# Performance work log

Measured on AMD Instinct MI355X. Metric: run time of the kernel, lower is better.

Reference implementation:

```python
import jax, jax.numpy as jnp
import numpy as np

N, C_IN, C_OUT, T, V = 128, 64, 64, 128, 25
GROUPS, K = 8, 3
REL = C_IN // 8  # rel_reduction=8, in_channels>16


def setup_inputs() -> dict:
    key = jax.random.key(0)
    ks = jax.random.split(key, 16)
    f = lambda k, sh, s=0.05: (jax.random.normal(k, sh) * s).astype(jnp.float32)
    return {
        "x0": jax.random.normal(ks[0], (N, C_IN, T, V), jnp.float32),
        "DecoupleA": f(ks[1], (K, GROUPS, V, V), 0.2),
        "A": f(ks[2], (K, V, V), 0.2),
        "alpha": jnp.full((1,), 0.5, jnp.float32),
        "w1": f(ks[3], (K, REL, C_IN)), "b1": f(ks[4], (K, REL)),
        "w2": f(ks[5], (K, REL, C_IN)), "b2": f(ks[6], (K, REL)),
        "w3": f(ks[7], (K, C_OUT, C_IN)), "b3": f(ks[8], (K, C_OUT)),
        "w4": f(ks[9], (K, C_OUT, REL)), "b4": f(ks[10], (K, C_OUT)),
        "Linear_weight": f(ks[11], (C_IN, C_OUT * K)),
        "Linear_bias": f(ks[12], (1, C_OUT * K, 1, 1)),
        "bn0_gamma": jnp.ones((C_OUT * K,), jnp.float32),
        "bn0_beta": jnp.zeros((C_OUT * K,), jnp.float32),
        "ens_w": f(ks[13], (C_OUT, 2 * C_OUT)), "ens_b": f(ks[14], (C_OUT,)),
        "bn_gamma": jnp.full((C_OUT,), 1e-6, jnp.float32),
        "bn_beta": jnp.zeros((C_OUT,), jnp.float32),
    }


def _bn(x, gamma, beta, eps=1e-5):
    # training-mode BatchNorm2d over NCHW: stats over (N, T, V)
    mu = x.mean(axis=(0, 2, 3), keepdims=True)
    var = x.var(axis=(0, 2, 3), keepdims=True)
    return (x - mu) * jax.lax.rsqrt(var + eps) * gamma[None, :, None, None] + beta[None, :, None, None]


def _norm_adj(A):
    # torch: D = A.sum(dim=rows) -> column sums; A @ diag(1/(D+1e-3)) scales columns
    d = A.sum(axis=-2)  # [..., V] column sums
    return A * (1.0 / (d + 0.001))[..., None, :]


def reference(x0, DecoupleA, A, alpha, w1, b1, w2, b2, w3, b3, w4, b4,
              Linear_weight, Linear_bias, bn0_gamma, bn0_beta, ens_w, ens_b,
              bn_gamma, bn_beta):
    n, c_in, t, v = x0.shape
    k, g = DecoupleA.shape[0], DecoupleA.shape[1]
    c_out = w3.shape[1]
    # DecoupleA.repeat(1, out_channels//groups, 1, 1) == tile along channel dim
    learn_A = jnp.tile(DecoupleA, (1, c_out // g, 1, 1))  # [K, C_OUT, V, V]
    norm_A = _norm_adj(learn_A)
    # decoupled linear path
    x = jnp.einsum('nctv,cd->ndtv', x0, Linear_weight) + Linear_bias
    x = _bn(x, bn0_gamma, bn0_beta)
    x = x.reshape(n, k, c_out, t, v)
    x = jnp.einsum('nkctv,kcvw->nctw', x, norm_A)  # [n, C_OUT, t, v]
    # CTRGC branches (conv-then-mean over T == mean-then-1x1 since conv is linear)
    xm = x0.mean(axis=2)  # [n, c_in, v]
    y = jnp.zeros((n, c_out, t, v), x0.dtype)
    for i in range(k):
        x1 = jnp.einsum('ncv,rc->nrv', xm, w1[i]) + b1[i][:, None]
        x2 = jnp.einsum('ncv,rc->nrv', xm, w2[i]) + b2[i][:, None]
        diff = jnp.tanh(x1[:, :, :, None] - x2[:, :, None, :])        # [n, rel, u, w]
        att = jnp.einsum('nruw,or->nouw', diff, w4[i]) + b4[i][None, :, None, None]
        att = att * alpha[0] + A[i][None, None]                        # [n, C_OUT, u, w]
        x3 = jnp.einsum('nctv,oc->notv', x0, w3[i]) + b3[i][None, :, None, None]
        y = y + jnp.einsum('ncuv,nctu->nctv', att, x3)
    cat = jnp.concatenate([x, y], axis=1)                              # [n, 2*C_OUT, t, v]
    out = jnp.einsum('nctv,oc->notv', cat, ens_w) + ens_b[None, :, None, None]
    out = _bn(out, bn_gamma, bn_beta)
    out = out + x0  # down is identity since in_channels == out_channels
    return jax.nn.relu(out)
```

## Files before the change

kernel.cpp:

```cpp
#include <hip/hip_runtime.h>
#include <cstddef>
#include <cstring>

typedef _Float16 h8 __attribute__((ext_vector_type(8)));
typedef _Float16 h4v __attribute__((ext_vector_type(4)));
typedef float f4 __attribute__((ext_vector_type(4)));
typedef unsigned int u32;
typedef unsigned short u16;

#define MTOT 409600.0f

#define DO_XM  15360000
#define DO_GP  15564800
#define DO_GR  16613376

#define WS_OB16 0
#define WS_ATT  13631488
#define WS_ATTB 23461888
#define WS_BN2P 23666688
#define WS_PAR  23827456
#define WS_CSN  23828000

#define ATT_H 27262976
#define NAB_H 47595520
#define WA_H  47622144
#define W3_H  47634432
#define EW_H  47646720

#define LDS_DYN 116736

__global__ __launch_bounds__(512) void k_gram(const float* __restrict__ x0,
                                              float* __restrict__ gp,
                                              const float* __restrict__ DA,
                                              const float* __restrict__ w3,
                                              const float* __restrict__ ensw,
                                              float* __restrict__ wsF) {
  int bid = blockIdx.x, tid = threadIdx.x;
  if (bid >= 256) {
    int pb = bid - 256;
    _Float16* wsH = (_Float16*)wsF;
    if (pb < 3) {
      if (tid < 200) {
        int k = pb, g = tid / 25, w = tid % 25;
        const float* base = DA + (k * 8 + g) * 625 + w;
        float s = 0.f;
        for (int v = 0; v < 25; v++) s += base[v * 25];
        float inv = 1.0f / (s + 0.001f);
        wsF[WS_CSN + k * 200 + g * 25 + w] = s * inv;
        _Float16* dst = wsH + NAB_H + (size_t)((k * 8 + g) * 32 + w) * 32;
        for (int v = 0; v < 25; v++) dst[v] = (_Float16)(base[v * 25] * inv);
        for (int v = 25; v < 32; v++) dst[v] = (_Float16)0.f;
      }
    } else if (pb == 3) {
      for (int idx = tid; idx < 5376; idx += 512) {
        int kg = idx / 224, r = idx % 224;
        int w = 25 + r / 32, v = r & 31;
        wsH[NAB_H + (size_t)(kg * 32 + w) * 32 + v] = (_Float16)0.f;
      }
    } else if (pb < 12) {
      int i0 = (pb - 4) * 1536;
      for (int i = tid; i < 1536; i += 512)
        wsH[W3_H + i0 + i] = (_Float16)w3[i0 + i];
    } else {
      int i0 = (pb - 12) * 2048;
      for (int i = tid; i < 2048; i += 512)
        wsH[EW_H + i0 + i] = (_Float16)ensw[i0 + i];
    }
    return;
  }
  __shared__ _Float16 Xs[64 * 128];
  char* smb = (char*)Xs;
  int n = bid >> 1, sh = bid & 1;
  int base = sh * 1536;
  int niter = sh ? 13 : 12;
  const float* xb = x0 + (size_t)n * 204800;
  int wid = tid >> 6, lane = tid & 63, l15 = lane & 15, l4 = lane >> 4;
  int ca = (wid & 3) * 16;
  int jb0 = (wid >> 2) * 2;
  f4 acc[2] = {{0.f, 0.f, 0.f, 0.f}, {0.f, 0.f, 0.f, 0.f}};
  int sc = tid >> 3, scol = (tid & 7) * 16;
  int swz = (sc & 7) << 4;
  for (int it = 0; it < niter; ++it) {
    int s0 = base + it * 128;
    __syncthreads();
    const float* src = xb + sc * 3200 + s0 + scol;
#pragma unroll
    for (int j = 0; j < 4; ++j) {
      float4 f = *(const float4*)(src + j * 4);
      h4v hv = {(_Float16)f.x, (_Float16)f.y, (_Float16)f.z, (_Float16)f.w};
      *(h4v*)(smb + sc * 256 + (((scol + j * 4) * 2) ^ swz)) = hv;
    }
    __syncthreads();
#pragma unroll
    for (int kk = 0; kk < 4; ++kk) {
      int kb = kk * 64 + l4 * 16;
      int arow = ca + l15;
      h8 af = *(const h8*)(smb + arow * 256 + (kb ^ ((arow & 7) << 4)));
#pragma unroll
      for (int j = 0; j < 2; ++j) {
        int brow = (jb0 + j) * 16 + l15;
        h8 bf = *(const h8*)(smb + brow * 256 + (kb ^ ((brow & 7) << 4)));
        acc[j] = __builtin_amdgcn_mfma_f32_16x16x32_f16(af, bf, acc[j], 0, 0, 0);
      }
    }
  }
  float* o = gp + (size_t)bid * 4096;
#pragma unroll
  for (int j = 0; j < 2; ++j)
#pragma unroll
    for (int q = 0; q < 4; ++q)
      o[(ca + l4 * 4 + q) * 64 + (jb0 + j) * 16 + l15] = acc[j][q];
}

__global__ __launch_bounds__(256) void k_gred(float* __restrict__ dsc) {
  int bid = blockIdx.x, tid = threadIdx.x;
  if (bid < 16) {
    int idx = bid * 256 + tid;
    const float* gp = dsc + DO_GP;
    float s0 = 0.f, s1 = 0.f, s2 = 0.f, s3 = 0.f;
    for (int b = 0; b < 256; b += 4) {
      s0 += gp[(size_t)b * 4096 + idx];
      s1 += gp[(size_t)(b + 1) * 4096 + idx];
      s2 += gp[(size_t)(b + 2) * 4096 + idx];
      s3 += gp[(size_t)(b + 3) * 4096 + idx];
    }
    dsc[DO_GR + idx] = (s0 + s1) + (s2 + s3);
  } else {
    __shared__ float red[64][5];
    int c = tid >> 2, j = tid & 3;
    float s = 0.f;
    for (int nn = j; nn < 128; nn += 4) {
      const float* xmp = dsc + DO_XM + (size_t)(nn * 64 + c) * 25;
      for (int v = 0; v < 25; ++v) s += xmp[v];
    }
    red[c][j] = s;
    __syncthreads();
    if (j == 0)
      dsc[DO_GR + 4096 + c] = 128.f * (red[c][0] + red[c][1] + red[c][2] + red[c][3]);
  }
}

__global__ __launch_bounds__(256) void k_xm(const float* __restrict__ x0,
                                            float* __restrict__ dsc) {
  __shared__ float red[8][32];
  int bid = blockIdx.x;
  int n = bid >> 6, c = bid & 63;
  int tid = threadIdx.x;
  int tq = tid >> 5, v = tid & 31;
  const float* xb = x0 + (size_t)(n * 64 + c) * 3200;
  float s = 0.f;
  if (v < 25) {
    for (int j = 0; j < 16; j++) s += xb[(tq + 8 * j) * 25 + v];
  }
  red[tq][v] = s;
  __syncthreads();
  if (tq == 0 && v < 25) {
    float tot = 0.f;
#pragma unroll
    for (int q = 0; q < 8; q++) tot += red[q][v];
    dsc[DO_XM + (size_t)(n * 64 + c) * 25 + v] = tot * (1.0f / 128.0f);
  }
}

__global__ __launch_bounds__(256) void k_bnstat(const float* __restrict__ dsc,
                                                const float* __restrict__ Lw,
                                                const float* __restrict__ g0,
                                                const float* __restrict__ b0,
                                                float* __restrict__ wsF) {
  __shared__ float Gsh[64 * 66];
  __shared__ float Ly[64][17];
  __shared__ float part[16][17];
  __shared__ float a1L[16];
  int bid = blockIdx.x, tid = threadIdx.x;
  int d0 = bid * 16, dl = tid >> 4, r = tid & 15, d = d0 + dl;
  for (int idx = tid; idx < 4096; idx += 256)
    Gsh[(idx >> 6) * 66 + (idx & 63)] = dsc[DO_GR + idx];
  for (int idx = tid; idx < 1024; idx += 256)
    Ly[idx >> 4][idx & 15] = Lw[(idx >> 4) * 192 + d0 + (idx & 15)];
  __syncthreads();
  float acc = 0.f;
#pragma unroll
  for (int cc = 0; cc < 4; ++cc) {
    int c = r * 4 + cc;
    float h = 0.f;
    for (int c2 = 0; c2 < 64; ++c2) h += Gsh[c * 66 + c2] * Ly[c2][dl];
    acc += Ly[c][dl] * h;
  }
  part[dl][r] = acc;
  __syncthreads();
  if (r == 0) {
    float ex2 = 0.f;
#pragma unroll
    for (int i = 0; i < 16; ++i) ex2 += part[dl][i];
    ex2 *= (1.0f / MTOT);
    float mu = 0.f;
    for (int c = 0; c < 64; ++c) mu += dsc[DO_GR + 4096 + c] * Ly[c][dl];
    mu *= (1.0f / MTOT);
    float var = ex2 - mu * mu;
    float a1 = g0[d] * rsqrtf(var + 1e-5f);
    float b1c = b0[d] - a1 * mu;
    wsF[WS_PAR + 128 + d] = a1;
    wsF[WS_PAR + 320 + d] = b1c;
    a1L[dl] = a1;
  }
  __syncthreads();
  _Float16* wsH = (_Float16*)wsF;
  int k = d >> 6, cg = d & 63;
  float a1v = a1L[dl];
#pragma unroll
  for (int j = 0; j < 4; ++j) {
    int e = r * 4 + j;
    wsH[WA_H + k * 4096 + cg * 64 + e] = (_Float16)(a1v * Lw[e * 192 + d]);
  }
}

__global__ __launch_bounds__(256) void k_att(const float* __restrict__ dsc,
    const float* __restrict__ w1, const float* __restrict__ b1,
    const float* __restrict__ w2, const float* __restrict__ b2,
    const float* __restrict__ w4, const float* __restrict__ b4,
    const float* __restrict__ Ag, const float* __restrict__ alpha,
    const float* __restrict__ b3, float* __restrict__ wsF) {
  __shared__ float xms[1600];
  __shared__ float x1s[200];
  __shared__ float x2s[200];
  __shared__ float Td[5000];
  int bid = blockIdx.x, tid = threadIdx.x;
  int n = bid / 3, i = bid % 3;
  for (int idx = tid; idx < 1600; idx += 256)
    xms[idx] = dsc[DO_XM + (size_t)n * 1600 + idx];
  __syncthreads();
  for (int idx = tid; idx < 400; idx += 256) {
    int r = (idx % 200) / 25, u = idx % 25;
    const float* wv = (idx < 200 ? w1 : w2) + (i * 8 + r) * 64;
    float acc = (idx < 200 ? b1 : b2)[i * 8 + r];
    for (int c = 0; c < 64; c++) acc += xms[c * 25 + u] * wv[c];
    if (idx < 200) x1s[r * 25 + u] = acc; else x2s[r * 25 + u] = acc;
  }
  __syncthreads();
  for (int idx = tid; idx < 5000; idx += 256) {
    int r = idx / 625, u = (idx % 625) / 25, w = idx % 25;
    Td[idx] = tanhf(x1s[r * 25 + u] - x2s[r * 25 + w]);
  }
  __syncthreads();
  float al = alpha[0];
  u32* attW = (u32*)wsF;
  for (int p = tid; p < 1600; p += 256) {
    int o = p / 25, w = p % 25;
    float w4r[8];
#pragma unroll
    for (int r = 0; r < 8; r++) w4r[r] = w4[(i * 64 + o) * 8 + r];
    float b4v = b4[i * 64 + o];
    const float* AgW = Ag + i * 625 + w;
    float asum = 0.f;
    size_t rowH = (size_t)ATT_H + ((size_t)((n * 3 + i) * 64 + o) * 25 + w) * 32;
    u32* row = attW + rowH / 2;
    for (int up = 0; up < 16; ++up) {
      u32 word = 0;
#pragma unroll
      for (int h = 0; h < 2; ++h) {
        int u = up * 2 + h;
        float v = 0.f;
        if (u < 25) {
          float acc = b4v;
#pragma unroll
          for (int r = 0; r < 8; r++) acc += w4r[r] * Td[r * 625 + u * 25 + w];
          v = al * acc + AgW[u * 25];
          asum += v;
        }
        union { _Float16 hf; u16 b; } cv;
        cv.hf = (_Float16)v;
        word |= ((u32)cv.b) << (16 * h);
      }
      row[up] = word;
    }
    atomicAdd(&wsF[WS_ATTB + (size_t)n * 1600 + p], b3[i * 64 + o] * asum);
  }
}

__device__ __forceinline__ void stageX(const float* __restrict__ xn, char* sm, int tid) {
  for (int uu = tid; uu < 6400; uu += 1024) {
    int cg = uu & 15, s = uu >> 4;
    int c0 = cg * 4;
    const float* p = xn + c0 * 3200 + s;
    float a = p[0], b = p[3200], c = p[6400], d = p[9600];
    h4v hv = {(_Float16)a, (_Float16)b, (_Float16)c, (_Float16)d};
    *(h4v*)(sm + s * 128 + ((c0 * 2) ^ ((s & 7) << 4))) = hv;
  }
}
__device__ __forceinline__ void zeroHpads(char* sm, int tid) {
  for (int idx = tid; idx < 7168; idx += 1024) {
    int c = idx / 112, r = idx % 112;
    int t = r / 7, u = 25 + r % 7;
    int hs = (((t & 3) ^ ((c >> 2) & 3)) << 4);
    *(_Float16*)(sm + 51200 + c * 1024 + t * 64 + ((u * 2) ^ hs)) = (_Float16)0.f;
  }
}
__device__ __forceinline__ void gemm64(const _Float16* __restrict__ Aw, char* sm,
                                       int mt, int nt0, int nt1, int lane) {
  int l15 = lane & 15, l4 = lane >> 4;
  h8 a0 = *(const h8*)(Aw + (mt * 16 + l15) * 64 + l4 * 8);
  h8 a1 = *(const h8*)(Aw + (mt * 16 + l15) * 64 + 32 + l4 * 8);
  int s = nt0 * 16 + l15;
  int t = s / 25, u = s - t * 25;
  int hsc = ((mt * 4 + l4) & 3) << 4;
  for (int nt = nt0; nt < nt1; ++nt) {
    int sw = (s & 7) << 4;
    const char* rb = sm + s * 128;
    h8 b0 = *(const h8*)(rb + ((l4 * 16) ^ sw));
    h8 b1 = *(const h8*)(rb + ((64 + l4 * 16) ^ sw));
    f4 acc = {0.f, 0.f, 0.f, 0.f};
    acc = __builtin_amdgcn_mfma_f32_16x16x32_f16(a0, b0, acc, 0, 0, 0);
    acc = __builtin_amdgcn_mfma_f32_16x16x32_f16(a1, b1, acc, 0, 0, 0);
    int hs = ((t & 3) << 4) ^ hsc;
    char* wb = sm + 51200 + (mt * 16 + l4 * 4) * 1024 + t * 64 + ((u * 2) ^ hs);
#pragma unroll
    for (int q = 0; q < 4; ++q)
      *(_Float16*)(wb + q * 1024) = (_Float16)acc[q];
    s += 16;
    u += 16;
    if (u >= 25) { u -= 25; ++t; }
  }
}

__global__ __launch_bounds__(1024, 4) void kAB(const float* __restrict__ x0,
                                               float* ws,
                                               const float* __restrict__ ensb) {
  extern __shared__ char sm[];
  __shared__ float redS[128];
  __shared__ float attBs[1600];
  __shared__ float cbS[1600];
  const _Float16* wsH = (const _Float16*)ws;
  int tid = threadIdx.x, bid = blockIdx.x;
  int lb = (bid & 7) * 128 + (bid >> 3);
  int n = lb >> 3, tile = lb & 7;
  int wid = tid >> 6, lane = tid & 63, l15 = lane & 15, l4 = lane >> 4;
  int mt = wid & 3, q4 = wid >> 2, g = wid & 7;
  int nt0 = q4 ? 1 + 6 * q4 : 0;
  int nt1 = q4 ? nt0 + 6 : 7;
  if (tid < 128) redS[tid] = 0.f;
  for (int idx = tid; idx < 1600; idx += 1024)
    attBs[idx] = ws[WS_ATTB + (size_t)n * 1600 + idx];
  for (int idx = tid; idx < 1600; idx += 1024) {
    int c = idx / 25, w = idx - c * 25;
    int gg = c & 7;
    float s = 0.f;
#pragma unroll
    for (int k = 0; k < 3; ++k)
      s += ws[WS_PAR + 320 + k * 64 + c] * ws[WS_CSN + k * 200 + gg * 25 + w];
    cbS[idx] = s;
  }
  stageX(x0 + (size_t)n * 204800 + tile * 400, sm, tid);
  zeroHpads(sm, tid);
  __syncthreads();
  f4 accx[4][2], accy[4][2];
#pragma unroll
  for (int a = 0; a < 4; a++)
#pragma unroll
    for (int b = 0; b < 2; b++) {
      accx[a][b] = (f4){0.f, 0.f, 0.f, 0.f};
      accy[a][b] = (f4){0.f, 0.f, 0.f, 0.f};
    }
  for (int k = 0; k < 3; ++k) {
    gemm64(wsH + WA_H + k * 4096, sm, mt, nt0, nt1, lane);
    __syncthreads();
#pragma unroll
    for (int mt2 = 0; mt2 < 4; ++mt2) {
      int c = mt2 * 16 + wid;
      int hs = (((l15 & 3) ^ ((c >> 2) & 3)) << 4);
      h8 aH = *(const h8*)(sm + 51200 + c * 1024 + l15 * 64 + ((l4 * 16) ^ hs));
#pragma unroll
      for (int nt2 = 0; nt2 < 2; ++nt2) {
        const _Float16* nb = wsH + NAB_H +
            (size_t)((k * 8 + g) * 32 + nt2 * 16 + l15) * 32 + l4 * 8;
        accx[mt2][nt2] = __builtin_amdgcn_mfma_f32_16x16x32_f16(
            aH, *(const h8*)nb, accx[mt2][nt2], 0, 0, 0);
      }
    }
    __syncthreads();
  }
  for (int i = 0; i < 3; ++i) {
    gemm64(wsH + W3_H + i * 4096, sm, mt, nt0, nt1, lane);
    __syncthreads();
#pragma unroll
    for (int mt2 = 0; mt2 < 4; ++mt2) {
      int c = mt2 * 16 + wid;
      int hs = (((l15 & 3) ^ ((c >> 2) & 3)) << 4);
      h8 aX = *(const h8*)(sm + 51200 + c * 1024 + l15 * 64 + ((l4 * 16) ^ hs));
#pragma unroll
      for (int nt2 = 0; nt2 < 2; ++nt2) {
        int v = nt2 * 16 + l15;
        int vc = v < 25 ? v : 0;
        const _Float16* ab = wsH + ATT_H +
            ((size_t)((n * 3 + i) * 64 + c) * 25 + vc) * 32 + l4 * 8;
        accy[mt2][nt2] = __builtin_amdgcn_mfma_f32_16x16x32_f16(
            aX, *(const h8*)ab, accy[mt2][nt2], 0, 0, 0);
      }
    }
    __syncthreads();
  }
#pragma unroll
  for (int mt2 = 0; mt2 < 4; ++mt2) {
    int c = mt2 * 16 + wid;
#pragma unroll
    for (int nt2 = 0; nt2 < 2; ++nt2) {
      int w = nt2 * 16 + l15;
      if (w < 25) {
        float cbv = cbS[c * 25 + w];
        float abv = attBs[c * 25 + w];
#pragma unroll
        for (int q = 0; q < 4; ++q) {
          int t = l4 * 4 + q;
          int s = t * 25 + w;
          int sw = (s & 7) << 4;
          *(_Float16*)(sm + s * 256 + ((c * 2) ^ sw)) =
              (_Float16)(accx[mt2][nt2][q] + cbv);
          *(_Float16*)(sm + s * 256 + (((64 + c) * 2) ^ sw)) =
              (_Float16)(accy[mt2][nt2][q] + abv);
        }
      }
    }
  }
  __syncthreads();
  h8 ea[4];
#pragma unroll
  for (int ks = 0; ks < 4; ++ks)
    ea[ks] = *(const h8*)(wsH + EW_H + (mt * 16 + l15) * 128 + ks * 32 + l4 * 8);
  float eb[4];
#pragma unroll
  for (int q = 0; q < 4; ++q) eb[q] = ensb[mt * 16 + l4 * 4 + q];
  float lsum[4] = {0.f, 0.f, 0.f, 0.f}, lss[4] = {0.f, 0.f, 0.f, 0.f};
  u16* ob16 = (u16*)ws;
  for (int nt = nt0; nt < nt1; ++nt) {
    int s = nt * 16 + l15;
    int sw = (s & 7) << 4;
    f4 acc = {0.f, 0.f, 0.f, 0.f};
#pragma unroll
    for (int ks = 0; ks < 4; ++ks) {
      h8 b = *(const h8*)(sm + s * 256 + (((ks * 32 + l4 * 8) * 2) ^ sw));
      acc = __builtin_amdgcn_mfma_f32_16x16x32_f16(ea[ks], b, acc, 0, 0, 0);
    }
    size_t ob = (size_t)n * 204800 + (size_t)tile * 400 + s;
#pragma unroll
    for (int q = 0; q < 4; ++q) {
      int o = mt * 16 + l4 * 4 + q;
      union { _Float16 hf; u16 b; } cv;
      cv.hf = (_Float16)(acc[q] + eb[q]);
      ob16[ob + (size_t)o * 3200] = cv.b;
      float val = (float)cv.hf;
      lsum[q] += val;
      lss[q] += val * val;
    }
  }
#pragma unroll
  for (int q = 0; q < 4; ++q) {
#pragma unroll
    for (int d = 1; d < 16; d <<= 1) {
      lsum[q] += __shfl_xor(lsum[q], d);
      lss[q] += __shfl_xor(lss[q], d);
    }
  }
  if (l15 == 0) {
#pragma unroll
    for (int q = 0; q < 4; ++q) {
      int o = mt * 16 + l4 * 4 + q;
      atomicAdd(&redS[o], lsum[q]);
      atomicAdd(&redS[64 + o], lss[q]);
    }
  }
  __syncthreads();
  if (tid < 64) {
    ws[WS_BN2P + (size_t)bid * 128 + tid * 2] = redS[tid];
    ws[WS_BN2P + (size_t)bid * 128 + tid * 2 + 1] = redS[64 + tid];
  }
}

__global__ __launch_bounds__(256) void k_bn2(const float* __restrict__ g2,
                                             const float* __restrict__ b2,
                                             float* __restrict__ ws) {
  __shared__ float rs[256], rss[256];
  int o = blockIdx.x, tid = threadIdx.x;
  float s = 0.f, ss = 0.f;
  for (int b = tid; b < 1024; b += 256) {
    s += ws[WS_BN2P + (size_t)b * 128 + o * 2];
    ss += ws[WS_BN2P + (size_t)b * 128 + o * 2 + 1];
  }
  rs[tid] = s; rss[tid] = ss;
  __syncthreads();
  for (int st = 128; st > 0; st >>= 1) {
    if (tid < st) { rs[tid] += rs[tid + st]; rss[tid] += rss[tid + st]; }
    __syncthreads();
  }
  if (tid == 0) {
    float mu = rs[0] / MTOT;
    float var = rss[0] / MTOT - mu * mu;
    float a2 = g2[o] * rsqrtf(var + 1e-5f);
    ws[WS_PAR + o] = a2;
    ws[WS_PAR + 64 + o] = b2[o] - a2 * mu;
  }
}

__global__ __launch_bounds__(256) void k_final(const float* __restrict__ x0,
                                               const float* __restrict__ ws,
                                               float* __restrict__ dout) {
  size_t g = (size_t)blockIdx.x * 256 + threadIdx.x;
  h4v p = reinterpret_cast<const h4v*>(ws)[g];
  float4 x = reinterpret_cast<const float4*>(x0)[g];
  int o = (int)((g * 4 / 3200) & 63);
  float a2 = ws[WS_PAR + o], bc = ws[WS_PAR + 64 + o];
  float4 r;
  r.x = fmaxf(fmaf(a2, (float)p[0], bc) + x.x, 0.f);
  r.y = fmaxf(fmaf(a2, (float)p[1], bc) + x.y, 0.f);
  r.z = fmaxf(fmaf(a2, (float)p[2], bc) + x.z, 0.f);
  r.w = fmaxf(fmaf(a2, (float)p[3], bc) + x.w, 0.f);
  reinterpret_cast<float4*>(dout)[g] = r;
}

extern "C" void kernel_launch(void* const* d_in, const int* in_sizes, int n_in,
                              void* d_out, int out_size, void* d_ws, size_t ws_size,
                              hipStream_t stream) {
  const float* x0    = (const float*)d_in[0];
  const float* DA    = (const float*)d_in[1];
  const float* Ag    = (const float*)d_in[2];
  const float* alpha = (const float*)d_in[3];
  const float* w1    = (const float*)d_in[4];
  const float* b1    = (const float*)d_in[5];
  const float* w2    = (const float*)d_in[6];
  const float* b2    = (const float*)d_in[7];
  const float* w3    = (const float*)d_in[8];
  const float* b3    = (const float*)d_in[9];
  const float* w4    = (const float*)d_in[10];
  const float* b4    = (const float*)d_in[11];
  const float* Lw    = (const float*)d_in[12];
  const float* g0    = (const float*)d_in[14];
  const float* b0    = (const float*)d_in[15];
  const float* ensw  = (const float*)d_in[16];
  const float* ensb  = (const float*)d_in[17];
  const float* g2    = (const float*)d_in[18];
  const float* b2n   = (const float*)d_in[19];
  float* out = (float*)d_out;
  float* ws  = (float*)d_ws;

  hipFuncSetAttribute((const void*)kAB, hipFuncAttributeMaxDynamicSharedMemorySize, LDS_DYN);

  hipMemsetAsync(ws + WS_ATTB, 0, 204800 * sizeof(float), stream);
  k_xm<<<8192, 256, 0, stream>>>(x0, out);
  k_gram<<<272, 512, 0, stream>>>(x0, out + DO_GP, DA, w3, ensw, ws);
  k_att<<<384, 256, 0, stream>>>(out, w1, b1, w2, b2, w4, b4, Ag, alpha, b3, ws);
  k_gred<<<17, 256, 0, stream>>>(out);
  k_bnstat<<<12, 256, 0, stream>>>(out, Lw, g0, b0, ws);
  kAB<<<1024, 1024, LDS_DYN, stream>>>(x0, ws, ensb);
  k_bn2<<<64, 256, 0, stream>>>(g2, b2n, ws);
  k_final<<<25600, 256, 0, stream>>>(x0, ws, out);
}
```

Baseline: 320.4 us.

## Fuse per-sample time-mean into gram kernel via LDS atomics

Removes the separate k_xm kernel, which re-read all of x0 to compute the mean over T, and instead accumulates the mean inside k_gram while x0 tiles are already being loaded. Each block builds partial sums in LDS with atomics and then atomically adds them to global memory, which needs an extra memset of the output region. The stageX loop is also remapped so consecutive threads walk the spatial index within a channel group, giving more coalesced global reads. The cost is many LDS atomics inside the gram load loop and global atomics, whose float summation order is nondeterministic.

After: 411.3 us. 1.28x slower.

```diff
diff --git a/kernel.cpp b/kernel.cpp
--- a/kernel.cpp
+++ b/kernel.cpp
@@ -30,7 +30,7 @@
 #define LDS_DYN 116736
 
 __global__ __launch_bounds__(512) void k_gram(const float* __restrict__ x0,
-                                              float* __restrict__ gp,
+                                              float* __restrict__ dsc,
                                               const float* __restrict__ DA,
                                               const float* __restrict__ w3,
                                               const float* __restrict__ ensw,
@@ -69,6 +69,7 @@
     return;
   }
   __shared__ _Float16 Xs[64 * 128];
+  __shared__ float xmL[1600];
   char* smb = (char*)Xs;
   int n = bid >> 1, sh = bid & 1;
   int base = sh * 1536;
@@ -80,16 +81,30 @@
   f4 acc[2] = {{0.f, 0.f, 0.f, 0.f}, {0.f, 0.f, 0.f, 0.f}};
   int sc = tid >> 3, scol = (tid & 7) * 16;
   int swz = (sc & 7) << 4;
+  for (int idx = tid; idx < 1600; idx += 512) xmL[idx] = 0.f;
+  int vbase = (base + scol) % 25;
+  __syncthreads();
   for (int it = 0; it < niter; ++it) {
     int s0 = base + it * 128;
     __syncthreads();
     const float* src = xb + sc * 3200 + s0 + scol;
+    float* xrow = &xmL[sc * 25];
 #pragma unroll
     for (int j = 0; j < 4; ++j) {
       float4 f = *(const float4*)(src + j * 4);
       h4v hv = {(_Float16)f.x, (_Float16)f.y, (_Float16)f.z, (_Float16)f.w};
       *(h4v*)(smb + sc * 256 + (((scol + j * 4) * 2) ^ swz)) = hv;
-    }
+      int v0 = vbase + 4 * j;
+      int va = v0;      if (va >= 25) va -= 25;
+      int vb = v0 + 1;  if (vb >= 25) vb -= 25;
+      int vc2 = v0 + 2; if (vc2 >= 25) vc2 -= 25;
+      int vd = v0 + 3;  if (vd >= 25) vd -= 25;
+      atomicAdd(&xrow[va], f.x);
+      atomicAdd(&xrow[vb], f.y);
+      atomicAdd(&xrow[vc2], f.z);
+      atomicAdd(&xrow[vd], f.w);
+    }
+    vbase += 3; if (vbase >= 25) vbase -= 25;
     __syncthreads();
 #pragma unroll
     for (int kk = 0; kk < 4; ++kk) {
@@ -104,12 +119,15 @@
       }
     }
   }
-  float* o = gp + (size_t)bid * 4096;
+  float* o = dsc + DO_GP + (size_t)bid * 4096;
 #pragma unroll
   for (int j = 0; j < 2; ++j)
 #pragma unroll
     for (int q = 0; q < 4; ++q)
       o[(ca + l4 * 4 + q) * 64 + (jb0 + j) * 16 + l15] = acc[j][q];
+  __syncthreads();
+  for (int idx = tid; idx < 1600; idx += 512)
+    atomicAdd(&dsc[DO_XM + (size_t)n * 1600 + idx], xmL[idx] * (1.0f / 128.0f));
 }
 
 __global__ __launch_bounds__(256) void k_gred(float* __restrict__ dsc) {
@@ -137,28 +155,6 @@
     __syncthreads();
     if (j == 0)
       dsc[DO_GR + 4096 + c] = 128.f * (red[c][0] + red[c][1] + red[c][2] + red[c][3]);
-  }
-}
-
-__global__ __launch_bounds__(256) void k_xm(const float* __restrict__ x0,
-                                            float* __restrict__ dsc) {
-  __shared__ float red[8][32];
-  int bid = blockIdx.x;
-  int n = bid >> 6, c = bid & 63;
-  int tid = threadIdx.x;
-  int tq = tid >> 5, v = tid & 31;
-  const float* xb = x0 + (size_t)(n * 64 + c) * 3200;
-  float s = 0.f;
-  if (v < 25) {
-    for (int j = 0; j < 16; j++) s += xb[(tq + 8 * j) * 25 + v];
-  }
-  red[tq][v] = s;
-  __syncthreads();
-  if (tq == 0 && v < 25) {
-    float tot = 0.f;
-#pragma unroll
-    for (int q = 0; q < 8; q++) tot += red[q][v];
-    dsc[DO_XM + (size_t)(n * 64 + c) * 25 + v] = tot * (1.0f / 128.0f);
   }
 }
 
@@ -278,8 +274,8 @@
 }
 
 __device__ __forceinline__ void stageX(const float* __restrict__ xn, char* sm, int tid) {
-  for (int uu = tid; uu < 6400; uu += 1024) {
-    int cg = uu & 15, s = uu >> 4;
+  for (int u = tid; u < 6400; u += 1024) {
+    int cg = u / 400, s = u - cg * 400;
     int c0 = cg * 4;
     const float* p = xn + c0 * 3200 + s;
     float a = p[0], b = p[3200], c = p[6400], d = p[9600];
@@ -543,8 +539,8 @@
   hipFuncSetAttribute((const void*)kAB, hipFuncAttributeMaxDynamicSharedMemorySize, LDS_DYN);
 
   hipMemsetAsync(ws + WS_ATTB, 0, 204800 * sizeof(float), stream);
-  k_xm<<<8192, 256, 0, stream>>>(x0, out);
-  k_gram<<<272, 512, 0, stream>>>(x0, out + DO_GP, DA, w3, ensw, ws);
+  hipMemsetAsync(out + DO_XM, 0, 204800 * sizeof(float), stream);
+  k_gram<<<272, 512, 0, stream>>>(x0, out, DA, w3, ensw, ws);
   k_att<<<384, 256, 0, stream>>>(out, w1, b1, w2, b2, w4, b4, Ag, alpha, b3, ws);
   k_gred<<<17, 256, 0, stream>>>(out);
   k_bnstat<<<12, 256, 0, stream>>>(out, Lw, g0, b0, ws);
```

## Split Gram kernel across more blocks, hoist global operand loads in kAB

Applied to the files above, without the earlier changes.

The Gram-matrix kernel now splits each sample over 8 blocks with strided chunks instead of 2, so 1024 blocks fill the GPU instead of 256. The partial-sum reduction grows to 1024 partials, and the scratch offset moves to fit them. In the fused kernel, the normalized-adjacency and attention B-operands and the ensemble weights are loaded from global memory before the GEMM and barrier, so their latency overlaps the compute. stageX changes its index mapping so consecutive threads read contiguous spatial positions, giving coalesced global loads but possibly more LDS bank conflicts. The cost is four times as much partial-sum traffic and extra registers for the hoisted operands.

After: 342.7 us. +7.0%, slower.

```diff
diff --git a/kernel.cpp b/kernel.cpp
--- a/kernel.cpp
+++ b/kernel.cpp
@@ -12,7 +12,7 @@
 
 #define DO_XM  15360000
 #define DO_GP  15564800
-#define DO_GR  16613376
+#define DO_GR  19759104
 
 #define WS_OB16 0
 #define WS_ATT  13631488
@@ -30,14 +30,14 @@
 #define LDS_DYN 116736
 
 __global__ __launch_bounds__(512) void k_gram(const float* __restrict__ x0,
-                                              float* __restrict__ gp,
+                                              float* __restrict__ dsc,
                                               const float* __restrict__ DA,
                                               const float* __restrict__ w3,
                                               const float* __restrict__ ensw,
                                               float* __restrict__ wsF) {
   int bid = blockIdx.x, tid = threadIdx.x;
-  if (bid >= 256) {
-    int pb = bid - 256;
+  if (bid >= 1024) {
+    int pb = bid - 1024;
     _Float16* wsH = (_Float16*)wsF;
     if (pb < 3) {
       if (tid < 200) {
@@ -70,9 +70,7 @@
   }
   __shared__ _Float16 Xs[64 * 128];
   char* smb = (char*)Xs;
-  int n = bid >> 1, sh = bid & 1;
-  int base = sh * 1536;
-  int niter = sh ? 13 : 12;
+  int n = bid >> 3, part = bid & 7;
   const float* xb = x0 + (size_t)n * 204800;
   int wid = tid >> 6, lane = tid & 63, l15 = lane & 15, l4 = lane >> 4;
   int ca = (wid & 3) * 16;
@@ -80,8 +78,8 @@
   f4 acc[2] = {{0.f, 0.f, 0.f, 0.f}, {0.f, 0.f, 0.f, 0.f}};
   int sc = tid >> 3, scol = (tid & 7) * 16;
   int swz = (sc & 7) << 4;
-  for (int it = 0; it < niter; ++it) {
-    int s0 = base + it * 128;
+  for (int it = part; it < 25; it += 8) {
+    int s0 = it * 128;
     __syncthreads();
     const float* src = xb + sc * 3200 + s0 + scol;
 #pragma unroll
@@ -104,7 +102,7 @@
       }
     }
   }
-  float* o = gp + (size_t)bid * 4096;
+  float* o = dsc + DO_GP + (size_t)bid * 4096;
 #pragma unroll
   for (int j = 0; j < 2; ++j)
 #pragma unroll
@@ -118,7 +116,7 @@
     int idx = bid * 256 + tid;
     const float* gp = dsc + DO_GP;
     float s0 = 0.f, s1 = 0.f, s2 = 0.f, s3 = 0.f;
-    for (int b = 0; b < 256; b += 4) {
+    for (int b = 0; b < 1024; b += 4) {
       s0 += gp[(size_t)b * 4096 + idx];
       s1 += gp[(size_t)(b + 1) * 4096 + idx];
       s2 += gp[(size_t)(b + 2) * 4096 + idx];
@@ -278,8 +276,8 @@
 }
 
 __device__ __forceinline__ void stageX(const float* __restrict__ xn, char* sm, int tid) {
-  for (int uu = tid; uu < 6400; uu += 1024) {
-    int cg = uu & 15, s = uu >> 4;
+  for (int u = tid; u < 6400; u += 1024) {
+    int cg = u / 400, s = u - cg * 400;
     int c0 = cg * 4;
     const float* p = xn + c0 * 3200 + s;
     float a = p[0], b = p[3200], c = p[6400], d = p[9600];
@@ -361,6 +359,8 @@
       accy[a][b] = (f4){0.f, 0.f, 0.f, 0.f};
     }
   for (int k = 0; k < 3; ++k) {
+    h8 nb0 = *(const h8*)(wsH + NAB_H + (size_t)((k * 8 + g) * 32 + l15) * 32 + l4 * 8);
+    h8 nb1 = *(const h8*)(wsH + NAB_H + (size_t)((k * 8 + g) * 32 + 16 + l15) * 32 + l4 * 8);
     gemm64(wsH + WA_H + k * 4096, sm, mt, nt0, nt1, lane);
     __syncthreads();
 #pragma unroll
@@ -368,17 +368,24 @@
       int c = mt2 * 16 + wid;
       int hs = (((l15 & 3) ^ ((c >> 2) & 3)) << 4);
       h8 aH = *(const h8*)(sm + 51200 + c * 1024 + l15 * 64 + ((l4 * 16) ^ hs));
+      accx[mt2][0] = __builtin_amdgcn_mfma_f32_16x16x32_f16(aH, nb0, accx[mt2][0], 0, 0, 0);
+      accx[mt2][1] = __builtin_amdgcn_mfma_f32_16x16x32_f16(aH, nb1, accx[mt2][1], 0, 0, 0);
+    }
+    __syncthreads();
+  }
+  for (int i = 0; i < 3; ++i) {
+    h8 abr[4][2];
+#pragma unroll
+    for (int mt2 = 0; mt2 < 4; ++mt2) {
+      int c = mt2 * 16 + wid;
 #pragma unroll
       for (int nt2 = 0; nt2 < 2; ++nt2) {
-        const _Float16* nb = wsH + NAB_H +
-            (size_t)((k * 8 + g) * 32 + nt2 * 16 + l15) * 32 + l4 * 8;
-        accx[mt2][nt2] = __builtin_amdgcn_mfma_f32_16x16x32_f16(
-            aH, *(const h8*)nb, accx[mt2][nt2], 0, 0, 0);
+        int v = nt2 * 16 + l15;
+        int vc = v < 25 ? v : 0;
+        abr[mt2][nt2] = *(const h8*)(wsH + ATT_H +
+            ((size_t)((n * 3 + i) * 64 + c) * 25 + vc) * 32 + l4 * 8);
       }
     }
-    __syncthreads();
-  }
-  for (int i = 0; i < 3; ++i) {
     gemm64(wsH + W3_H + i * 4096, sm, mt, nt0, nt1, lane);
     __syncthreads();
 #pragma unroll
@@ -387,17 +394,19 @@
       int hs = (((l15 & 3) ^ ((c >> 2) & 3)) << 4);
       h8 aX = *(const h8*)(sm + 51200 + c * 1024 + l15 * 64 + ((l4 * 16) ^ hs));
 #pragma unroll
-      for (int nt2 = 0; nt2 < 2; ++nt2) {
-        int v = nt2 * 16 + l15;
-        int vc = v < 25 ? v : 0;
-        const _Float16* ab = wsH + ATT_H +
-            ((size_t)((n * 3 + i) * 64 + c) * 25 + vc) * 32 + l4 * 8;
+      for (int nt2 = 0; nt2 < 2; ++nt2)
         accy[mt2][nt2] = __builtin_amdgcn_mfma_f32_16x16x32_f16(
-            aX, *(const h8*)ab, accy[mt2][nt2], 0, 0, 0);
-      }
-    }
-    __syncthreads();
-  }
+            aX, abr[mt2][nt2], accy[mt2][nt2], 0, 0, 0);
+    }
+    __syncthreads();
+  }
+  h8 ea[4];
+#pragma unroll
+  for (int ks = 0; ks < 4; ++ks)
+    ea[ks] = *(const h8*)(wsH + EW_H + (mt * 16 + l15) * 128 + ks * 32 + l4 * 8);
+  float eb[4];
+#pragma unroll
+  for (int q = 0; q < 4; ++q) eb[q] = ensb[mt * 16 + l4 * 4 + q];
 #pragma unroll
   for (int mt2 = 0; mt2 < 4; ++mt2) {
     int c = mt2 * 16 + wid;
@@ -421,13 +430,6 @@
     }
   }
   __syncthreads();
-  h8 ea[4];
-#pragma unroll
-  for (int ks = 0; ks < 4; ++ks)
-    ea[ks] = *(const h8*)(wsH + EW_H + (mt * 16 + l15) * 128 + ks * 32 + l4 * 8);
-  float eb[4];
-#pragma unroll
-  for (int q = 0; q < 4; ++q) eb[q] = ensb[mt * 16 + l4 * 4 + q];
   float lsum[4] = {0.f, 0.f, 0.f, 0.f}, lss[4] = {0.f, 0.f, 0.f, 0.f};
   u16* ob16 = (u16*)ws;
   for (int nt = nt0; nt < nt1; ++nt) {
@@ -544,7 +546,7 @@
 
   hipMemsetAsync(ws + WS_ATTB, 0, 204800 * sizeof(float), stream);
   k_xm<<<8192, 256, 0, stream>>>(x0, out);
-  k_gram<<<272, 512, 0, stream>>>(x0, out + DO_GP, DA, w3, ensw, ws);
+  k_gram<<<1040, 512, 0, stream>>>(x0, out, DA, w3, ensw, ws);
   k_att<<<384, 256, 0, stream>>>(out, w1, b1, w2, b2, w4, b4, Ag, alpha, b3, ws);
   k_gred<<<17, 256, 0, stream>>>(out);
   k_bnstat<<<12, 256, 0, stream>>>(out, Lw, g0, b0, ws);
```
